# Optimization experiments

Hardware: AMD Instinct MI355X
Metric: run time of the kernel (lower is better)

## Reference

```python
import jax, jax.numpy as jnp
import numpy as np

B, T, D, H, E, TOPK = 4, 1024, 1024, 16, 8, 2
DH = D // H
FF = 4 * D
EPS = 1e-9


def setup_inputs() -> dict:
    key = jax.random.key(0)
    ks = jax.random.split(key, 8)
    s = 0.02
    return {
        "x": jax.random.normal(ks[0], (B, T, D), jnp.float32),
        "c": jax.random.normal(ks[1], (B, 1, D), jnp.float32),
        "ln1_w": jnp.ones((D,), jnp.float32),
        "w_qkv": jax.random.normal(ks[2], (3 * D, D), jnp.float32) * s,
        "w_proj": jax.random.normal(ks[3], (D, D), jnp.float32) * s,
        "ln2_w": jnp.ones((D,), jnp.float32),
        "router_w": jax.random.normal(ks[4], (E, D), jnp.float32) * s,
        "expert_w1": jax.random.normal(ks[5], (E, FF, D), jnp.float32) * s,
        "expert_w2": jax.random.normal(ks[6], (E, D, FF), jnp.float32) * s,
    }


def _layernorm(x, w):
    mu = jnp.mean(x, axis=-1, keepdims=True)
    var = jnp.mean(jnp.square(x - mu), axis=-1, keepdims=True)
    return (x - mu) * jax.lax.rsqrt(var + 1e-5) * w


def reference(x, c, ln1_w, w_qkv, w_proj, ln2_w, router_w, expert_w1, expert_w2):
    # --- causal self-attention with AdaLN-style additive conditioning ---
    h = _layernorm(x, ln1_w) + c                          # [B,T,D]
    qkv = jnp.einsum('btd,ed->bte', h, w_qkv)             # [B,T,3D]
    q, k, v = jnp.split(qkv, 3, axis=-1)
    q = q.reshape(B, T, H, DH).transpose(0, 2, 1, 3)       # [B,H,T,dh]
    k = k.reshape(B, T, H, DH).transpose(0, 2, 1, 3)
    v = v.reshape(B, T, H, DH).transpose(0, 2, 1, 3)
    scores = jnp.einsum('bhqd,bhkd->bhqk', q, k) / jnp.sqrt(jnp.float32(DH))
    causal = jnp.tril(jnp.ones((T, T), bool))
    scores = jnp.where(causal, scores, jnp.float32(-1e30))
    attn = jax.nn.softmax(scores, axis=-1)
    o = jnp.einsum('bhqk,bhkd->bhqd', attn, v)
    o = o.transpose(0, 2, 1, 3).reshape(B, T, D)
    x = x + jnp.einsum('btd,ed->bte', o, w_proj)

    # --- pre-MoE LayerNorm (note: module overwrites x with ln_2(x)) ---
    x = _layernorm(x, ln2_w)

    # --- router (non-cond path): linear, max-shift, softmax, eps clamp, top-k ---
    logits = jnp.einsum('btd,ed->bte', x, router_w)        # [B,T,E]
    logits = logits - jnp.max(logits, axis=-1, keepdims=True)
    probs = jax.nn.softmax(logits, axis=-1)
    probs = jnp.clip(probs + EPS, EPS, 1.0 - EPS)
    _, top_idx = jax.lax.top_k(probs, TOPK)                # [B,T,k]
    mask = jnp.sum(jax.nn.one_hot(top_idx, E, dtype=probs.dtype), axis=-2)  # [B,T,E]
    router_probs = mask * probs
    router_probs = router_probs / jnp.sum(router_probs, axis=-1, keepdims=True)

    # --- experts: GPT MLP per expert (fc -> GELU -> proj), combine by probs ---
    # Dense-compute form is mathematically identical: router_probs is 0 for
    # non-selected experts, so masked gather/scatter == weighted dense sum.
    hid = jax.nn.gelu(jnp.einsum('btd,efd->btef', x, expert_w1), approximate=False)
    expert_out = jnp.einsum('btef,edf->bted', hid, expert_w2)  # [B,T,E,D]
    next_states = jnp.einsum('bted,bte->btd', expert_out, router_probs)

    return x + next_states
```

## Files before the change

### kernel.cpp

```cpp
#include <hip/hip_runtime.h>
#include <cstdint>
#include <cstddef>


#define AS1 __attribute__((address_space(1)))
#define AS3 __attribute__((address_space(3)))

typedef unsigned short u16;
typedef __attribute__((ext_vector_type(8))) short short8;
typedef __attribute__((ext_vector_type(8))) _Float16 half8;
typedef __attribute__((ext_vector_type(4))) float f32x4;

constexpr int Bc = 4, Tc = 1024, Dc = 1024, Hc = 16, Ec = 8, FFc = 4096;
constexpr int Mtok = Bc * Tc;

constexpr size_t PS_WQKV = (size_t)3 * Dc * Dc;
constexpr size_t PS_WPROJ = (size_t)Dc * Dc;
constexpr size_t PS_H = (size_t)Mtok * Dc;

constexpr float LO_SCALE = 4096.0f;
constexpr float LO_INV = 1.0f / 4096.0f;

__device__ __forceinline__ u16 f2bf(float f) {
  unsigned u = __float_as_uint(f);
  u += 0x7fffu + ((u >> 16) & 1u);
  return (u16)(u >> 16);
}
__device__ __forceinline__ float bf2f(u16 v) { return __uint_as_float(((unsigned)v) << 16); }
__device__ __forceinline__ u16 f2h(float f) {
  _Float16 h = (_Float16)f;
  return *(u16*)&h;
}
__device__ __forceinline__ float h2f(u16 v) {
  _Float16 h = *(_Float16*)&v;
  return (float)h;
}
__device__ __forceinline__ float gelu_f(float v) {
  return 0.5f * v * (1.0f + erff(v * 0.70710678118654752440f));
}

__global__ __launch_bounds__(256) void cvt_fp16_kernel(const float* __restrict__ in,
                                                       u16* __restrict__ out, int n4) {
  int i = blockIdx.x * 256 + threadIdx.x;
  if (i >= n4) return;
  float4 v = reinterpret_cast<const float4*>(in)[i];
  uint2 o;
  o.x = (unsigned)f2h(v.x) | ((unsigned)f2h(v.y) << 16);
  o.y = (unsigned)f2h(v.z) | ((unsigned)f2h(v.w) << 16);
  reinterpret_cast<uint2*>(out)[i] = o;
}

__global__ __launch_bounds__(256) void split2h_kernel(const float* __restrict__ in,
                                                      u16* __restrict__ out,
                                                      size_t ps, int n4) {
  int i = blockIdx.x * 256 + threadIdx.x;
  if (i >= n4) return;
  float4 v = reinterpret_cast<const float4*>(in)[i];
  float a[4] = {v.x, v.y, v.z, v.w};
  unsigned h[4], lo[4];
#pragma unroll
  for (int j = 0; j < 4; ++j) {
    u16 hh = f2h(a[j]);
    float r = (a[j] - h2f(hh)) * LO_SCALE;
    h[j] = hh; lo[j] = f2h(r);
  }
  uint2 o0, o1;
  o0.x = h[0] | (h[1] << 16);   o0.y = h[2] | (h[3] << 16);
  o1.x = lo[0] | (lo[1] << 16); o1.y = lo[2] | (lo[3] << 16);
  const size_t base = (size_t)i * 4;
  *(uint2*)&out[base] = o0;
  *(uint2*)&out[ps + base] = o1;
}

__global__ __launch_bounds__(256) void ln1_kernel(const float* __restrict__ x,
                                                  const float* __restrict__ w,
                                                  const float* __restrict__ c,
                                                  u16* __restrict__ hp) {
  const int row = blockIdx.x, tid = threadIdx.x;
  const int b = row >> 10;
  const float4 v = reinterpret_cast<const float4*>(x + (size_t)row * Dc)[tid];
  __shared__ float red[256];
  red[tid] = v.x + v.y + v.z + v.w;
  __syncthreads();
  for (int s = 128; s > 0; s >>= 1) { if (tid < s) red[tid] += red[tid + s]; __syncthreads(); }
  const float mu = red[0] * (1.0f / Dc);
  __syncthreads();
  const float dx = v.x - mu, dy = v.y - mu, dz = v.z - mu, dw = v.w - mu;
  red[tid] = dx * dx + dy * dy + dz * dz + dw * dw;
  __syncthreads();
  for (int s = 128; s > 0; s >>= 1) { if (tid < s) red[tid] += red[tid + s]; __syncthreads(); }
  const float rs = rsqrtf(red[0] * (1.0f / Dc) + 1e-5f);
  const float4 wv = reinterpret_cast<const float4*>(w)[tid];
  const float4 cv = reinterpret_cast<const float4*>(c + (size_t)b * Dc)[tid];
  float a[4];
  a[0] = dx * rs * wv.x + cv.x; a[1] = dy * rs * wv.y + cv.y;
  a[2] = dz * rs * wv.z + cv.z; a[3] = dw * rs * wv.w + cv.w;
  unsigned h[4], lo[4];
#pragma unroll
  for (int j = 0; j < 4; ++j) {
    u16 hh = f2h(a[j]);
    float r = (a[j] - h2f(hh)) * LO_SCALE;
    h[j] = hh; lo[j] = f2h(r);
  }
  uint2 o0, o1;
  o0.x = h[0] | (h[1] << 16);   o0.y = h[2] | (h[3] << 16);
  o1.x = lo[0] | (lo[1] << 16); o1.y = lo[2] | (lo[3] << 16);
  const size_t base = (size_t)row * Dc + tid * 4;
  *(uint2*)&hp[base] = o0;
  *(uint2*)&hp[PS_H + base] = o1;
}

__global__ __launch_bounds__(256) void ln2_kernel(const float* __restrict__ xin,
                                                  const float* __restrict__ w,
                                                  float* __restrict__ xf,
                                                  u16* __restrict__ xb) {
  const int row = blockIdx.x, tid = threadIdx.x;
  const float4 v = reinterpret_cast<const float4*>(xin + (size_t)row * Dc)[tid];
  __shared__ float red[256];
  red[tid] = v.x + v.y + v.z + v.w;
  __syncthreads();
  for (int s = 128; s > 0; s >>= 1) { if (tid < s) red[tid] += red[tid + s]; __syncthreads(); }
  const float mu = red[0] * (1.0f / Dc);
  __syncthreads();
  const float dx = v.x - mu, dy = v.y - mu, dz = v.z - mu, dw = v.w - mu;
  red[tid] = dx * dx + dy * dy + dz * dz + dw * dw;
  __syncthreads();
  for (int s = 128; s > 0; s >>= 1) { if (tid < s) red[tid] += red[tid + s]; __syncthreads(); }
  const float rs = rsqrtf(red[0] * (1.0f / Dc) + 1e-5f);
  const float4 wv = reinterpret_cast<const float4*>(w)[tid];
  float4 ov;
  ov.x = dx * rs * wv.x; ov.y = dy * rs * wv.y; ov.z = dz * rs * wv.z; ov.w = dw * rs * wv.w;
  reinterpret_cast<float4*>(xf + (size_t)row * Dc)[tid] = ov;
  uint2 o;
  o.x = (unsigned)f2h(ov.x) | ((unsigned)f2h(ov.y) << 16);
  o.y = (unsigned)f2h(ov.z) | ((unsigned)f2h(ov.w) << 16);
  reinterpret_cast<uint2*>(xb + (size_t)row * Dc)[tid] = o;
}

__device__ __forceinline__ void stage4(const u16* a0, const u16* a1,
                                       const u16* b0, const u16* b1,
                                       u16* buf, int lds0) {
  __builtin_amdgcn_global_load_lds((AS1 void*)a0, (AS3 void*)(buf + lds0), 16, 0, 0);
  __builtin_amdgcn_global_load_lds((AS1 void*)a1, (AS3 void*)(buf + 2048 + lds0), 16, 0, 0);
  __builtin_amdgcn_global_load_lds((AS1 void*)b0, (AS3 void*)(buf + 4096 + lds0), 16, 0, 0);
  __builtin_amdgcn_global_load_lds((AS1 void*)b1, (AS3 void*)(buf + 6144 + lds0), 16, 0, 0);
}
__device__ __forceinline__ void stage8(const u16* ah0, const u16* ah1,
                                       const u16* al0, const u16* al1,
                                       const u16* bh0, const u16* bh1,
                                       const u16* bl0, const u16* bl1,
                                       u16* buf, int lds0) {
  __builtin_amdgcn_global_load_lds((AS1 void*)ah0, (AS3 void*)(buf + lds0), 16, 0, 0);
  __builtin_amdgcn_global_load_lds((AS1 void*)ah1, (AS3 void*)(buf + 2048 + lds0), 16, 0, 0);
  __builtin_amdgcn_global_load_lds((AS1 void*)al0, (AS3 void*)(buf + 4096 + lds0), 16, 0, 0);
  __builtin_amdgcn_global_load_lds((AS1 void*)al1, (AS3 void*)(buf + 6144 + lds0), 16, 0, 0);
  __builtin_amdgcn_global_load_lds((AS1 void*)bh0, (AS3 void*)(buf + 8192 + lds0), 16, 0, 0);
  __builtin_amdgcn_global_load_lds((AS1 void*)bh1, (AS3 void*)(buf + 10240 + lds0), 16, 0, 0);
  __builtin_amdgcn_global_load_lds((AS1 void*)bl0, (AS3 void*)(buf + 12288 + lds0), 16, 0, 0);
  __builtin_amdgcn_global_load_lds((AS1 void*)bl1, (AS3 void*)(buf + 14336 + lds0), 16, 0, 0);
}

__device__ __forceinline__ void gemm_f16_core(const u16* a0, const u16* a1,
                                              const u16* b0, const u16* b1,
                                              int K, u16* S, f32x4 acc[4][4]) {
  const int tid = threadIdx.x;
  const int lane = tid & 63;
  const int wave = tid >> 6;
  const int wm = (wave & 1) * 64;
  const int wn = (wave >> 1) * 64;
  const int frow = lane & 15;
  const int gs = ((lane >> 4) ^ ((frow >> 1) & 3)) * 8;
  int aoff[4], boff[4];
#pragma unroll
  for (int t = 0; t < 4; ++t) {
    aoff[t] = (wm + t * 16 + frow) * 32 + gs;
    boff[t] = 4096 + (wn + t * 16 + frow) * 32 + gs;
  }
  const int lds0 = tid * 8;
  stage4(a0, a1, b0, b1, S, lds0);
  a0 += 32; a1 += 32; b0 += 32; b1 += 32;
  int cur = 0;
  for (int k0 = 0; k0 < K; k0 += 32) {
    __syncthreads();
    if (k0 + 32 < K) {
      stage4(a0, a1, b0, b1, S + (cur ^ 1) * 8192, lds0);
      a0 += 32; a1 += 32; b0 += 32; b1 += 32;
    }
    const u16* As = S + cur * 8192;
    half8 af[4], bfr[4];
#pragma unroll
    for (int t = 0; t < 4; ++t) af[t] = *(const half8*)(As + aoff[t]);
#pragma unroll
    for (int t = 0; t < 4; ++t) bfr[t] = *(const half8*)(As + boff[t]);
#pragma unroll
    for (int mt = 0; mt < 4; ++mt)
#pragma unroll
      for (int nt = 0; nt < 4; ++nt)
        acc[mt][nt] = __builtin_amdgcn_mfma_f32_16x16x32_f16(af[mt], bfr[nt], acc[mt][nt], 0, 0, 0);
    cur ^= 1;
  }
}

__device__ __forceinline__ void gemm_f16s2_core(const u16* ah0, const u16* ah1,
                                                const u16* al0, const u16* al1,
                                                const u16* bh0, const u16* bh1,
                                                const u16* bl0, const u16* bl1,
                                                int K, u16* S,
                                                f32x4 acc0[4][4], f32x4 acc1[4][4]) {
  const int tid = threadIdx.x;
  const int lane = tid & 63;
  const int wave = tid >> 6;
  const int wm = (wave & 1) * 64;
  const int wn = (wave >> 1) * 64;
  const int frow = lane & 15;
  const int gs = ((lane >> 4) ^ ((frow >> 1) & 3)) * 8;
  int aoff[4], boff[4];
#pragma unroll
  for (int t = 0; t < 4; ++t) {
    aoff[t] = (wm + t * 16 + frow) * 32 + gs;
    boff[t] = 8192 + (wn + t * 16 + frow) * 32 + gs;
  }
  const int lds0 = tid * 8;
  stage8(ah0, ah1, al0, al1, bh0, bh1, bl0, bl1, S, lds0);
  ah0 += 32; ah1 += 32; al0 += 32; al1 += 32;
  bh0 += 32; bh1 += 32; bl0 += 32; bl1 += 32;
  int cur = 0;
  for (int k0 = 0; k0 < K; k0 += 32) {
    __syncthreads();
    if (k0 + 32 < K) {
      stage8(ah0, ah1, al0, al1, bh0, bh1, bl0, bl1, S + (cur ^ 1) * 16384, lds0);
      ah0 += 32; ah1 += 32; al0 += 32; al1 += 32;
      bh0 += 32; bh1 += 32; bl0 += 32; bl1 += 32;
    }
    const u16* Sb = S + cur * 16384;
    half8 ahf[4], bhf[4];
#pragma unroll
    for (int t = 0; t < 4; ++t) {
      ahf[t] = *(const half8*)(Sb + aoff[t]);
      bhf[t] = *(const half8*)(Sb + boff[t]);
    }
#pragma unroll
    for (int mt = 0; mt < 4; ++mt)
#pragma unroll
      for (int nt = 0; nt < 4; ++nt)
        acc0[mt][nt] = __builtin_amdgcn_mfma_f32_16x16x32_f16(ahf[mt], bhf[nt], acc0[mt][nt], 0, 0, 0);
    {
      half8 alf[4];
#pragma unroll
      for (int t = 0; t < 4; ++t) alf[t] = *(const half8*)(Sb + 4096 + aoff[t]);
#pragma unroll
      for (int mt = 0; mt < 4; ++mt)
#pragma unroll
        for (int nt = 0; nt < 4; ++nt)
          acc1[mt][nt] = __builtin_amdgcn_mfma_f32_16x16x32_f16(alf[mt], bhf[nt], acc1[mt][nt], 0, 0, 0);
    }
    {
      half8 blf[4];
#pragma unroll
      for (int t = 0; t < 4; ++t) blf[t] = *(const half8*)(Sb + 4096 + boff[t]);
#pragma unroll
      for (int mt = 0; mt < 4; ++mt)
#pragma unroll
        for (int nt = 0; nt < 4; ++nt)
          acc1[mt][nt] = __builtin_amdgcn_mfma_f32_16x16x32_f16(ahf[mt], blf[nt], acc1[mt][nt], 0, 0, 0);
    }
    cur ^= 1;
  }
}

__global__ __launch_bounds__(256) void gemm_qkv_kernel(const u16* __restrict__ A,
                                                       const u16* __restrict__ Bw,
                                                       float* __restrict__ Cout) {
  __shared__ u16 S[2 * 16384];
  const int bn = blockIdx.x, bm = blockIdx.y, tid = threadIdx.x;
  const int r = tid >> 2, kk = ((tid & 3) ^ ((r >> 1) & 3)) * 8;
  const u16* ah0 = A + (size_t)(bm * 128 + r) * 1024 + kk;
  const u16* ah1 = ah0 + (size_t)64 * 1024;
  const u16* bh0 = Bw + (size_t)(bn * 128 + r) * 1024 + kk;
  const u16* bh1 = bh0 + (size_t)64 * 1024;
  f32x4 acc0[4][4] = {}, acc1[4][4] = {};
  gemm_f16s2_core(ah0, ah1, ah0 + PS_H, ah1 + PS_H,
                  bh0, bh1, bh0 + PS_WQKV, bh1 + PS_WQKV,
                  1024, S, acc0, acc1);
  const int lane = tid & 63, wave = tid >> 6;
  const int wm = (wave & 1) * 64, wn = (wave >> 1) * 64;
  const int col = lane & 15, rb = (lane >> 4) * 4;
#pragma unroll
  for (int mt = 0; mt < 4; ++mt)
#pragma unroll
    for (int rr = 0; rr < 4; ++rr) {
      const int m = bm * 128 + wm + mt * 16 + rb + rr;
#pragma unroll
      for (int nt = 0; nt < 4; ++nt) {
        const int n = bn * 128 + wn + nt * 16 + col;
        Cout[(size_t)m * 3072 + n] = acc0[mt][nt][rr] + acc1[mt][nt][rr] * LO_INV;
      }
    }
}

__global__ __launch_bounds__(256) void gemm_proj_kernel(const u16* __restrict__ A,
                                                        const u16* __restrict__ Bw,
                                                        const float* __restrict__ xres,
                                                        float* __restrict__ xmid) {
  __shared__ u16 S[2 * 16384];
  const int bn = blockIdx.x, bm = blockIdx.y, tid = threadIdx.x;
  const int r = tid >> 2, kk = ((tid & 3) ^ ((r >> 1) & 3)) * 8;
  const u16* ah0 = A + (size_t)(bm * 128 + r) * 1024 + kk;
  const u16* ah1 = ah0 + (size_t)64 * 1024;
  const u16* bh0 = Bw + (size_t)(bn * 128 + r) * 1024 + kk;
  const u16* bh1 = bh0 + (size_t)64 * 1024;
  f32x4 acc0[4][4] = {}, acc1[4][4] = {};
  gemm_f16s2_core(ah0, ah1, ah0 + PS_H, ah1 + PS_H,
                  bh0, bh1, bh0 + PS_WPROJ, bh1 + PS_WPROJ,
                  1024, S, acc0, acc1);
  const int lane = tid & 63, wave = tid >> 6;
  const int wm = (wave & 1) * 64, wn = (wave >> 1) * 64;
  const int col = lane & 15, rb = (lane >> 4) * 4;
#pragma unroll
  for (int mt = 0; mt < 4; ++mt)
#pragma unroll
    for (int rr = 0; rr < 4; ++rr) {
      const int m = bm * 128 + wm + mt * 16 + rb + rr;
#pragma unroll
      for (int nt = 0; nt < 4; ++nt) {
        const int n = bn * 128 + wn + nt * 16 + col;
        xmid[(size_t)m * 1024 + n] =
            xres[(size_t)m * 1024 + n] + acc0[mt][nt][rr] + acc1[mt][nt][rr] * LO_INV;
      }
    }
}

__global__ __launch_bounds__(256, 3) void attn_mfma_kernel(const float* __restrict__ qkv,
                                                           float* __restrict__ obuf) {
  constexpr int KS = 72;
  constexpr int PSt = 68;
  __shared__ u16 Kh[64 * KS], Klo[64 * KS];
  __shared__ u16 Vh[64 * KS], Vlo[64 * KS];
  __shared__ u16 Ph[4][16 * PSt], Pl[4][16 * PSt];

  const int tid = threadIdx.x, lane = tid & 63, w = tid >> 6;
  const int lr = lane & 15, g = lane >> 4;
  const int bh = blockIdx.y, b = bh >> 4, h = bh & 15;
  const int blk = blockIdx.x;
  const int qrow = blk * 64 + w * 16 + lr;

  short8 qh[2], ql[2];
  {
    const float* qp = qkv + (size_t)(b * Tc + qrow) * 3072 + h * 64 + g * 8;
    const float4 f0 = *(const float4*)(qp);
    const float4 f1 = *(const float4*)(qp + 4);
    const float4 f2 = *(const float4*)(qp + 32);
    const float4 f3 = *(const float4*)(qp + 36);
    const float qq[16] = {f0.x, f0.y, f0.z, f0.w, f1.x, f1.y, f1.z, f1.w,
                          f2.x, f2.y, f2.z, f2.w, f3.x, f3.y, f3.z, f3.w};
#pragma unroll
    for (int s = 0; s < 2; ++s)
#pragma unroll
      for (int j = 0; j < 8; ++j) {
        const float v = qq[s * 8 + j] * 0.125f;
        const u16 hi = f2bf(v);
        qh[s][j] = (short)hi;
        ql[s][j] = (short)f2bf(v - bf2f(hi));
      }
  }

  const int tkl = (tid & 31) * 2;
  const int td0 = (tid >> 5) * 8;
  const float* kgb = qkv + (size_t)b * Tc * 3072 + 1024 + h * 64;
  const float* vgb = kgb + 1024;

  f32x4 oacc[4] = {};
  float mrun = -1e30f, lrun = 0.f;

  for (int c = 0; c <= blk; ++c) {
    const int k0 = c * 64;
    __syncthreads();
    {
      const float* kr0 = kgb + (size_t)(k0 + tkl) * 3072 + td0;
      const float* kr1 = kr0 + 3072;
      const float* vr0 = vgb + (size_t)(k0 + tkl) * 3072 + td0;
      const float* vr1 = vr0 + 3072;
      const float4 ka0 = *(const float4*)kr0, ka1 = *(const float4*)(kr0 + 4);
      const float4 kb0 = *(const float4*)kr1, kb1 = *(const float4*)(kr1 + 4);
      const float4 va0 = *(const float4*)vr0, va1 = *(const float4*)(vr0 + 4);
      const float4 vb0 = *(const float4*)vr1, vb1 = *(const float4*)(vr1 + 4);
      const float ka[8] = {ka0.x, ka0.y, ka0.z, ka0.w, ka1.x, ka1.y, ka1.z, ka1.w};
      const float kb[8] = {kb0.x, kb0.y, kb0.z, kb0.w, kb1.x, kb1.y, kb1.z, kb1.w};
      const float va[8] = {va0.x, va0.y, va0.z, va0.w, va1.x, va1.y, va1.z, va1.w};
      const float vb[8] = {vb0.x, vb0.y, vb0.z, vb0.w, vb1.x, vb1.y, vb1.z, vb1.w};
      short8 kh0, kl0, kh1, kl1;
#pragma unroll
      for (int j = 0; j < 8; ++j) {
        const u16 h0 = f2bf(ka[j]); kh0[j] = (short)h0; kl0[j] = (short)f2bf(ka[j] - bf2f(h0));
        const u16 h1 = f2bf(kb[j]); kh1[j] = (short)h1; kl1[j] = (short)f2bf(kb[j] - bf2f(h1));
      }
      *(short8*)(Kh + tkl * KS + td0) = kh0;
      *(short8*)(Kh + (tkl + 1) * KS + td0) = kh1;
      *(short8*)(Klo + tkl * KS + td0) = kl0;
      *(short8*)(Klo + (tkl + 1) * KS + td0) = kl1;
#pragma unroll
      for (int i = 0; i < 8; ++i) {
        const u16 h0 = f2bf(va[i]); const u16 l0 = f2bf(va[i] - bf2f(h0));
        const u16 h1 = f2bf(vb[i]); const u16 l1 = f2bf(vb[i] - bf2f(h1));
        *(unsigned*)(Vh + (td0 + i) * KS + tkl) = (unsigned)h0 | ((unsigned)h1 << 16);
        *(unsigned*)(Vlo + (td0 + i) * KS + tkl) = (unsigned)l0 | ((unsigned)l1 << 16);
      }
    }
    __syncthreads();

    f32x4 sacc[4] = {};
#pragma unroll
    for (int kt = 0; kt < 4; ++kt) {
      const u16* kap = Kh + (kt * 16 + lr) * KS + g * 8;
      const u16* klp = Klo + (kt * 16 + lr) * KS + g * 8;
      const short8 ah0 = *(const short8*)kap;
      const short8 ah1 = *(const short8*)(kap + 32);
      const short8 al0 = *(const short8*)klp;
      const short8 al1 = *(const short8*)(klp + 32);
      sacc[kt] = __builtin_amdgcn_mfma_f32_16x16x32_bf16(ah0, qh[0], sacc[kt], 0, 0, 0);
      sacc[kt] = __builtin_amdgcn_mfma_f32_16x16x32_bf16(al0, qh[0], sacc[kt], 0, 0, 0);
      sacc[kt] = __builtin_amdgcn_mfma_f32_16x16x32_bf16(ah0, ql[0], sacc[kt], 0, 0, 0);
      sacc[kt] = __builtin_amdgcn_mfma_f32_16x16x32_bf16(ah1, qh[1], sacc[kt], 0, 0, 0);
      sacc[kt] = __builtin_amdgcn_mfma_f32_16x16x32_bf16(al1, qh[1], sacc[kt], 0, 0, 0);
      sacc[kt] = __builtin_amdgcn_mfma_f32_16x16x32_bf16(ah1, ql[1], sacc[kt], 0, 0, 0);
    }

    if (c == blk) {
#pragma unroll
      for (int kt = 0; kt < 4; ++kt)
#pragma unroll
        for (int r = 0; r < 4; ++r)
          if (k0 + kt * 16 + g * 4 + r > qrow) sacc[kt][r] = -1e30f;
    }

    float mt = -1e30f;
#pragma unroll
    for (int kt = 0; kt < 4; ++kt)
#pragma unroll
      for (int r = 0; r < 4; ++r) mt = fmaxf(mt, sacc[kt][r]);
    mt = fmaxf(mt, __shfl_xor(mt, 16));
    mt = fmaxf(mt, __shfl_xor(mt, 32));
    const float mnew = fmaxf(mrun, mt);
    const float alpha = __expf(mrun - mnew);
    float psum = 0.f;
    u16* php = Ph[w] + lr * PSt;
    u16* plp = Pl[w] + lr * PSt;
#pragma unroll
    for (int kt = 0; kt < 4; ++kt) {
      u16 hh[4], ll[4];
#pragma unroll
      for (int r = 0; r < 4; ++r) {
        const float p = __expf(sacc[kt][r] - mnew);
        psum += p;
        hh[r] = f2bf(p);
        ll[r] = f2bf(p - bf2f(hh[r]));
      }
      uint2 wh, wl;
      wh.x = (unsigned)hh[0] | ((unsigned)hh[1] << 16);
      wh.y = (unsigned)hh[2] | ((unsigned)hh[3] << 16);
      wl.x = (unsigned)ll[0] | ((unsigned)ll[1] << 16);
      wl.y = (unsigned)ll[2] | ((unsigned)ll[3] << 16);
      *(uint2*)(php + kt * 16 + g * 4) = wh;
      *(uint2*)(plp + kt * 16 + g * 4) = wl;
    }
    psum += __shfl_xor(psum, 16);
    psum += __shfl_xor(psum, 32);
    mrun = mnew;
    lrun = lrun * alpha + psum;
#pragma unroll
    for (int dt = 0; dt < 4; ++dt) {
      oacc[dt][0] *= alpha; oacc[dt][1] *= alpha;
      oacc[dt][2] *= alpha; oacc[dt][3] *= alpha;
    }
    __syncthreads();

    const short8 pbh0 = *(const short8*)(php + g * 8);
    const short8 pbh1 = *(const short8*)(php + 32 + g * 8);
    const short8 pbl0 = *(const short8*)(plp + g * 8);
    const short8 pbl1 = *(const short8*)(plp + 32 + g * 8);
#pragma unroll
    for (int dt = 0; dt < 4; ++dt) {
      const u16* vap = Vh + (dt * 16 + lr) * KS + g * 8;
      const u16* vlp2 = Vlo + (dt * 16 + lr) * KS + g * 8;
      const short8 vh0 = *(const short8*)vap;
      const short8 vh1 = *(const short8*)(vap + 32);
      const short8 vl0 = *(const short8*)vlp2;
      const short8 vl1 = *(const short8*)(vlp2 + 32);
      oacc[dt] = __builtin_amdgcn_mfma_f32_16x16x32_bf16(vh0, pbh0, oacc[dt], 0, 0, 0);
      oacc[dt] = __builtin_amdgcn_mfma_f32_16x16x32_bf16(vl0, pbh0, oacc[dt], 0, 0, 0);
      oacc[dt] = __builtin_amdgcn_mfma_f32_16x16x32_bf16(vh0, pbl0, oacc[dt], 0, 0, 0);
      oacc[dt] = __builtin_amdgcn_mfma_f32_16x16x32_bf16(vh1, pbh1, oacc[dt], 0, 0, 0);
      oacc[dt] = __builtin_amdgcn_mfma_f32_16x16x32_bf16(vl1, pbh1, oacc[dt], 0, 0, 0);
      oacc[dt] = __builtin_amdgcn_mfma_f32_16x16x32_bf16(vh1, pbl1, oacc[dt], 0, 0, 0);
    }
  }

  const float invl = 1.0f / lrun;
  float* ob = obuf + (size_t)(b * Tc + qrow) * 1024 + h * 64;
#pragma unroll
  for (int dt = 0; dt < 4; ++dt) {
    float4 o4;
    o4.x = oacc[dt][0] * invl; o4.y = oacc[dt][1] * invl;
    o4.z = oacc[dt][2] * invl; o4.w = oacc[dt][3] * invl;
    *(float4*)(ob + dt * 16 + g * 4) = o4;
  }
}

__global__ __launch_bounds__(256) void router_kernel(const float* __restrict__ x2,
                                                     const float* __restrict__ rw,
                                                     int* __restrict__ cnt,
                                                     int* __restrict__ tok,
                                                     float* __restrict__ wt) {
  __shared__ float xr[1024];
  __shared__ float part[8][32];
  __shared__ float lg[8];
  const int row = blockIdx.x, tid = threadIdx.x;
  reinterpret_cast<float4*>(xr)[tid] = reinterpret_cast<const float4*>(x2 + (size_t)row * Dc)[tid];
  __syncthreads();
  const int e = tid >> 5, j = tid & 31;
  float p = 0.f;
  for (int d = j; d < Dc; d += 32) p += xr[d] * rw[e * Dc + d];
  part[e][j] = p;
  __syncthreads();
  if (tid < 8) {
    float s = 0.f;
    for (int q = 0; q < 32; ++q) s += part[tid][q];
    lg[tid] = s;
  }
  __syncthreads();
  if (tid == 0) {
    int i0 = 0;
    for (int q = 1; q < 8; ++q) if (lg[q] > lg[i0]) i0 = q;
    int i1 = (i0 == 0) ? 1 : 0;
    for (int q = 0; q < 8; ++q) if (q != i0 && lg[q] > lg[i1]) i1 = q;
    float mx = lg[0];
    for (int q = 1; q < 8; ++q) mx = fmaxf(mx, lg[q]);
    float ex[8], s = 0.f;
    for (int q = 0; q < 8; ++q) { ex[q] = expf(lg[q] - mx); s += ex[q]; }
    const float inv = 1.f / s;
    float p0v = fminf(fmaxf(ex[i0] * inv + 1e-9f, 1e-9f), 1.f - 1e-9f);
    float p1v = fminf(fmaxf(ex[i1] * inv + 1e-9f, 1e-9f), 1.f - 1e-9f);
    const float sw = 1.f / (p0v + p1v);
    int p0 = atomicAdd(&cnt[i0], 1);
    tok[i0 * Mtok + p0] = row; wt[i0 * Mtok + p0] = p0v * sw;
    int p1 = atomicAdd(&cnt[i1], 1);
    tok[i1 * Mtok + p1] = row; wt[i1 * Mtok + p1] = p1v * sw;
  }
}

__global__ __launch_bounds__(256) void gemm_e1_kernel(const u16* __restrict__ x2b,
                                                      const u16* __restrict__ w1,
                                                      const int* __restrict__ cnt,
                                                      const int* __restrict__ tok,
                                                      u16* __restrict__ hid) {
  const int bn = blockIdx.x;
  const int e = blockIdx.y >> 5, it = blockIdx.y & 31;
  const int n_e = cnt[e];
  if (it * 128 >= n_e) return;
  int offs = 0;
  for (int q = 0; q < 8; ++q) offs += (q < e) ? cnt[q] : 0;
  __shared__ u16 S[2 * 8192];
  const int tid = threadIdx.x;
  const int r = tid >> 2, kk = ((tid & 3) ^ ((r >> 1) & 3)) * 8;
  const int i0 = it * 128 + r, i1 = i0 + 64;
  const int t0 = tok[e * Mtok + ((i0 < n_e) ? i0 : (n_e - 1))];
  const int t1 = tok[e * Mtok + ((i1 < n_e) ? i1 : (n_e - 1))];
  const u16* a0 = x2b + (size_t)t0 * 1024 + kk;
  const u16* a1 = x2b + (size_t)t1 * 1024 + kk;
  const u16* b0 = w1 + (size_t)e * FFc * Dc + (size_t)(bn * 128 + r) * 1024 + kk;
  const u16* b1 = b0 + (size_t)64 * 1024;
  f32x4 acc[4][4] = {};
  gemm_f16_core(a0, a1, b0, b1, 1024, S, acc);
  const int lane = tid & 63, wave = tid >> 6;
  const int wm = (wave & 1) * 64, wn = (wave >> 1) * 64;
  const int col = lane & 15, rb = (lane >> 4) * 4;
#pragma unroll
  for (int mt = 0; mt < 4; ++mt)
#pragma unroll
    for (int rr = 0; rr < 4; ++rr) {
      const int i = it * 128 + wm + mt * 16 + rb + rr;
      if (i < n_e) {
        const size_t hrow = (size_t)(offs + i) * FFc;
#pragma unroll
        for (int nt = 0; nt < 4; ++nt) {
          const int n = bn * 128 + wn + nt * 16 + col;
          hid[hrow + n] = f2h(gelu_f(acc[mt][nt][rr]));
        }
      }
    }
}

__global__ __launch_bounds__(256) void gemm_e2_kernel(const u16* __restrict__ hid,
                                                      const u16* __restrict__ w2,
                                                      const int* __restrict__ cnt,
                                                      const int* __restrict__ tok,
                                                      const float* __restrict__ wt,
                                                      float* __restrict__ out) {
  const int bn = blockIdx.x;
  const int e = blockIdx.y >> 5, it = blockIdx.y & 31;
  const int n_e = cnt[e];
  if (it * 128 >= n_e) return;
  int offs = 0;
  for (int q = 0; q < 8; ++q) offs += (q < e) ? cnt[q] : 0;
  __shared__ u16 S[2 * 8192];
  const int tid = threadIdx.x;
  const int r = tid >> 2, kk = ((tid & 3) ^ ((r >> 1) & 3)) * 8;
  const int i0 = it * 128 + r, i1 = i0 + 64;
  const int ri0 = offs + ((i0 < n_e) ? i0 : (n_e - 1));
  const int ri1 = offs + ((i1 < n_e) ? i1 : (n_e - 1));
  const u16* a0 = hid + (size_t)ri0 * FFc + kk;
  const u16* a1 = hid + (size_t)ri1 * FFc + kk;
  const u16* b0 = w2 + (size_t)e * Dc * FFc + (size_t)(bn * 128 + r) * FFc + kk;
  const u16* b1 = b0 + (size_t)64 * FFc;
  f32x4 acc[4][4] = {};
  gemm_f16_core(a0, a1, b0, b1, FFc, S, acc);
  const int lane = tid & 63, wave = tid >> 6;
  const int wm = (wave & 1) * 64, wn = (wave >> 1) * 64;
  const int col = lane & 15, rb = (lane >> 4) * 4;
#pragma unroll
  for (int mt = 0; mt < 4; ++mt)
#pragma unroll
    for (int rr = 0; rr < 4; ++rr) {
      const int i = it * 128 + wm + mt * 16 + rb + rr;
      if (i < n_e) {
        const int tk = tok[e * Mtok + i];
        const float wgt = wt[e * Mtok + i];
#pragma unroll
        for (int nt = 0; nt < 4; ++nt) {
          const int n = bn * 128 + wn + nt * 16 + col;
          atomicAdd(&out[(size_t)tk * 1024 + n], wgt * acc[mt][nt][rr]);
        }
      }
    }
}

constexpr size_t OFF_WQKV3 = 0;
constexpr size_t OFF_WPROJ3 = 18874368;
constexpr size_t OFF_W1 = 25165824;
constexpr size_t OFF_W2 = 92274688;
constexpr size_t OFF_HPL = 159383552;
constexpr size_t OFF_QKV = 184549376;
constexpr size_t OFF_OF = 234881024;
constexpr size_t OFF_X2 = 251658240;
constexpr size_t OFF_CNT = 260046848;
constexpr size_t OFF_TOK = OFF_CNT + 256;
constexpr size_t OFF_WTL = OFF_TOK + (size_t)Ec * Mtok * 4;

extern "C" void kernel_launch(void* const* d_in, const int* in_sizes, int n_in,
                              void* d_out, int out_size, void* d_ws, size_t ws_size,
                              hipStream_t stream) {
  const float* x = (const float*)d_in[0];
  const float* c = (const float*)d_in[1];
  const float* ln1_w = (const float*)d_in[2];
  const float* w_qkv = (const float*)d_in[3];
  const float* w_proj = (const float*)d_in[4];
  const float* ln2_w = (const float*)d_in[5];
  const float* router_w = (const float*)d_in[6];
  const float* ew1 = (const float*)d_in[7];
  const float* ew2 = (const float*)d_in[8];
  float* out = (float*)d_out;
  char* ws = (char*)d_ws;

  u16* wqkv2 = (u16*)(ws + OFF_WQKV3);
  u16* wproj2 = (u16*)(ws + OFF_WPROJ3);
  u16* w1_h = (u16*)(ws + OFF_W1);
  u16* w2_h = (u16*)(ws + OFF_W2);
  u16* hpl = (u16*)(ws + OFF_HPL);
  float* qkvf = (float*)(ws + OFF_QKV);
  float* of = (float*)(ws + OFF_OF);
  u16* x2_h = (u16*)(ws + OFF_X2);
  u16* hid_h = (u16*)(ws + OFF_QKV);
  int* cnt = (int*)(ws + OFF_CNT);
  int* tok = (int*)(ws + OFF_TOK);
  float* wtl = (float*)(ws + OFF_WTL);

  split2h_kernel<<<(3 * Dc * Dc / 4 + 255) / 256, 256, 0, stream>>>(w_qkv, wqkv2, PS_WQKV, 3 * Dc * Dc / 4);
  split2h_kernel<<<(Dc * Dc / 4 + 255) / 256, 256, 0, stream>>>(w_proj, wproj2, PS_WPROJ, Dc * Dc / 4);
  {
    int n4 = Ec * FFc * Dc / 4;
    cvt_fp16_kernel<<<(n4 + 255) / 256, 256, 0, stream>>>(ew1, w1_h, n4);
    cvt_fp16_kernel<<<(n4 + 255) / 256, 256, 0, stream>>>(ew2, w2_h, n4);
  }
  ln1_kernel<<<Mtok, 256, 0, stream>>>(x, ln1_w, c, hpl);
  gemm_qkv_kernel<<<dim3(24, 32), 256, 0, stream>>>(hpl, wqkv2, qkvf);
  attn_mfma_kernel<<<dim3(Tc / 64, Bc * Hc), 256, 0, stream>>>(qkvf, of);
  split2h_kernel<<<(Mtok * Dc / 4 + 255) / 256, 256, 0, stream>>>(of, hpl, PS_H, Mtok * Dc / 4);
  gemm_proj_kernel<<<dim3(8, 32), 256, 0, stream>>>(hpl, wproj2, x, of);
  ln2_kernel<<<Mtok, 256, 0, stream>>>(of, ln2_w, out, x2_h);
  (void)hipMemsetAsync(cnt, 0, Ec * sizeof(int), stream);
  router_kernel<<<Mtok, 256, 0, stream>>>(out, router_w, cnt, tok, wtl);
  gemm_e1_kernel<<<dim3(32, 256), 256, 0, stream>>>(x2_h, w1_h, cnt, tok, hid_h);
  gemm_e2_kernel<<<dim3(8, 256), 256, 0, stream>>>(hid_h, w2_h, cnt, tok, wtl, out);
}
```

Measured before the change: 943.5 us.

## Triple-buffer LDS in GEMM cores with vmcnt-based waits instead of syncthreads

Converts the double-buffered global_load_lds GEMM mainloops (plain f16 and split-f16) to a three-stage ring with two tiles in flight. Each iteration waits only for the oldest tile via s_waitcnt vmcnt(N) plus a barrier, rather than a full __syncthreads, so global loads can overlap more compute. LDS per block grows by half, which may lower occupancy for the QKV/proj kernels that now use 96KB.

Measured after the change: 946.7 us. No clear change (+0.3%).

```diff
diff --git a/kernel.cpp b/kernel.cpp
--- a/kernel.cpp
+++ b/kernel.cpp
@@ -160,6 +160,26 @@
   __builtin_amdgcn_global_load_lds((AS1 void*)bl1, (AS3 void*)(buf + 14336 + lds0), 16, 0, 0);
 }
 
+#define PIPE_WAIT(N)                                        \
+  asm volatile("s_waitcnt vmcnt(" #N ")" ::: "memory");     \
+  __builtin_amdgcn_s_barrier();                             \
+  asm volatile("" ::: "memory");                            \
+  __builtin_amdgcn_sched_barrier(0);
+
+__device__ __forceinline__ void gemm_f16_compute(const u16* Sb, const int aoff[4],
+                                                 const int boff[4], f32x4 acc[4][4]) {
+  half8 af[4], bfr[4];
+#pragma unroll
+  for (int t = 0; t < 4; ++t) af[t] = *(const half8*)(Sb + aoff[t]);
+#pragma unroll
+  for (int t = 0; t < 4; ++t) bfr[t] = *(const half8*)(Sb + boff[t]);
+#pragma unroll
+  for (int mt = 0; mt < 4; ++mt)
+#pragma unroll
+    for (int nt = 0; nt < 4; ++nt)
+      acc[mt][nt] = __builtin_amdgcn_mfma_f32_16x16x32_f16(af[mt], bfr[nt], acc[mt][nt], 0, 0, 0);
+}
+
 __device__ __forceinline__ void gemm_f16_core(const u16* a0, const u16* a1,
                                               const u16* b0, const u16* b1,
                                               int K, u16* S, f32x4 acc[4][4]) {
@@ -177,27 +197,59 @@
     boff[t] = 4096 + (wn + t * 16 + frow) * 32 + gs;
   }
   const int lds0 = tid * 8;
+  const int NT = K >> 5;
   stage4(a0, a1, b0, b1, S, lds0);
   a0 += 32; a1 += 32; b0 += 32; b1 += 32;
+  stage4(a0, a1, b0, b1, S + 8192, lds0);
+  a0 += 32; a1 += 32; b0 += 32; b1 += 32;
   int cur = 0;
-  for (int k0 = 0; k0 < K; k0 += 32) {
-    __syncthreads();
-    if (k0 + 32 < K) {
-      stage4(a0, a1, b0, b1, S + (cur ^ 1) * 8192, lds0);
+  for (int t = 0; t < NT - 1; ++t) {
+    PIPE_WAIT(4)
+    if (t + 2 < NT) {
+      int nxt = cur + 2; if (nxt >= 3) nxt -= 3;
+      stage4(a0, a1, b0, b1, S + nxt * 8192, lds0);
       a0 += 32; a1 += 32; b0 += 32; b1 += 32;
     }
-    const u16* As = S + cur * 8192;
-    half8 af[4], bfr[4];
-#pragma unroll
-    for (int t = 0; t < 4; ++t) af[t] = *(const half8*)(As + aoff[t]);
-#pragma unroll
-    for (int t = 0; t < 4; ++t) bfr[t] = *(const half8*)(As + boff[t]);
+    gemm_f16_compute(S + cur * 8192, aoff, boff, acc);
+    ++cur; if (cur >= 3) cur = 0;
+  }
+  PIPE_WAIT(0)
+  gemm_f16_compute(S + cur * 8192, aoff, boff, acc);
+}
+
+__device__ __forceinline__ void gemm_f16s2_compute(const u16* Sb, const int aoff[4],
+                                                   const int boff[4],
+                                                   f32x4 acc0[4][4], f32x4 acc1[4][4]) {
+  half8 ahf[4], bhf[4];
+#pragma unroll
+  for (int t = 0; t < 4; ++t) {
+    ahf[t] = *(const half8*)(Sb + aoff[t]);
+    bhf[t] = *(const half8*)(Sb + boff[t]);
+  }
+#pragma unroll
+  for (int mt = 0; mt < 4; ++mt)
+#pragma unroll
+    for (int nt = 0; nt < 4; ++nt)
+      acc0[mt][nt] = __builtin_amdgcn_mfma_f32_16x16x32_f16(ahf[mt], bhf[nt], acc0[mt][nt], 0, 0, 0);
+  {
+    half8 alf[4];
+#pragma unroll
+    for (int t = 0; t < 4; ++t) alf[t] = *(const half8*)(Sb + 4096 + aoff[t]);
 #pragma unroll
     for (int mt = 0; mt < 4; ++mt)
 #pragma unroll
       for (int nt = 0; nt < 4; ++nt)
-        acc[mt][nt] = __builtin_amdgcn_mfma_f32_16x16x32_f16(af[mt], bfr[nt], acc[mt][nt], 0, 0, 0);
-    cur ^= 1;
+        acc1[mt][nt] = __builtin_amdgcn_mfma_f32_16x16x32_f16(alf[mt], bhf[nt], acc1[mt][nt], 0, 0, 0);
+  }
+  {
+    half8 blf[4];
+#pragma unroll
+    for (int t = 0; t < 4; ++t) blf[t] = *(const half8*)(Sb + 4096 + boff[t]);
+#pragma unroll
+    for (int mt = 0; mt < 4; ++mt)
+#pragma unroll
+      for (int nt = 0; nt < 4; ++nt)
+        acc1[mt][nt] = __builtin_amdgcn_mfma_f32_16x16x32_f16(ahf[mt], blf[nt], acc1[mt][nt], 0, 0, 0);
   }
 }
 
@@ -221,57 +273,33 @@
     boff[t] = 8192 + (wn + t * 16 + frow) * 32 + gs;
   }
   const int lds0 = tid * 8;
+  const int NT = K >> 5;
   stage8(ah0, ah1, al0, al1, bh0, bh1, bl0, bl1, S, lds0);
   ah0 += 32; ah1 += 32; al0 += 32; al1 += 32;
   bh0 += 32; bh1 += 32; bl0 += 32; bl1 += 32;
+  stage8(ah0, ah1, al0, al1, bh0, bh1, bl0, bl1, S + 16384, lds0);
+  ah0 += 32; ah1 += 32; al0 += 32; al1 += 32;
+  bh0 += 32; bh1 += 32; bl0 += 32; bl1 += 32;
   int cur = 0;
-  for (int k0 = 0; k0 < K; k0 += 32) {
-    __syncthreads();
-    if (k0 + 32 < K) {
-      stage8(ah0, ah1, al0, al1, bh0, bh1, bl0, bl1, S + (cur ^ 1) * 16384, lds0);
+  for (int t = 0; t < NT - 1; ++t) {
+    PIPE_WAIT(8)
+    if (t + 2 < NT) {
+      int nxt = cur + 2; if (nxt >= 3) nxt -= 3;
+      stage8(ah0, ah1, al0, al1, bh0, bh1, bl0, bl1, S + nxt * 16384, lds0);
       ah0 += 32; ah1 += 32; al0 += 32; al1 += 32;
       bh0 += 32; bh1 += 32; bl0 += 32; bl1 += 32;
     }
-    const u16* Sb = S + cur * 16384;
-    half8 ahf[4], bhf[4];
-#pragma unroll
-    for (int t = 0; t < 4; ++t) {
-      ahf[t] = *(const half8*)(Sb + aoff[t]);
-      bhf[t] = *(const half8*)(Sb + boff[t]);
-    }
-#pragma unroll
-    for (int mt = 0; mt < 4; ++mt)
-#pragma unroll
-      for (int nt = 0; nt < 4; ++nt)
-        acc0[mt][nt] = __builtin_amdgcn_mfma_f32_16x16x32_f16(ahf[mt], bhf[nt], acc0[mt][nt], 0, 0, 0);
-    {
-      half8 alf[4];
-#pragma unroll
-      for (int t = 0; t < 4; ++t) alf[t] = *(const half8*)(Sb + 4096 + aoff[t]);
-#pragma unroll
-      for (int mt = 0; mt < 4; ++mt)
-#pragma unroll
-        for (int nt = 0; nt < 4; ++nt)
-          acc1[mt][nt] = __builtin_amdgcn_mfma_f32_16x16x32_f16(alf[mt], bhf[nt], acc1[mt][nt], 0, 0, 0);
-    }
-    {
-      half8 blf[4];
-#pragma unroll
-      for (int t = 0; t < 4; ++t) blf[t] = *(const half8*)(Sb + 4096 + boff[t]);
-#pragma unroll
-      for (int mt = 0; mt < 4; ++mt)
-#pragma unroll
-        for (int nt = 0; nt < 4; ++nt)
-          acc1[mt][nt] = __builtin_amdgcn_mfma_f32_16x16x32_f16(ahf[mt], blf[nt], acc1[mt][nt], 0, 0, 0);
-    }
-    cur ^= 1;
-  }
+    gemm_f16s2_compute(S + cur * 16384, aoff, boff, acc0, acc1);
+    ++cur; if (cur >= 3) cur = 0;
+  }
+  PIPE_WAIT(0)
+  gemm_f16s2_compute(S + cur * 16384, aoff, boff, acc0, acc1);
 }
 
 __global__ __launch_bounds__(256) void gemm_qkv_kernel(const u16* __restrict__ A,
                                                        const u16* __restrict__ Bw,
                                                        float* __restrict__ Cout) {
-  __shared__ u16 S[2 * 16384];
+  __shared__ u16 S[3 * 16384];
   const int bn = blockIdx.x, bm = blockIdx.y, tid = threadIdx.x;
   const int r = tid >> 2, kk = ((tid & 3) ^ ((r >> 1) & 3)) * 8;
   const u16* ah0 = A + (size_t)(bm * 128 + r) * 1024 + kk;
@@ -302,7 +330,7 @@
                                                         const u16* __restrict__ Bw,
                                                         const float* __restrict__ xres,
                                                         float* __restrict__ xmid) {
-  __shared__ u16 S[2 * 16384];
+  __shared__ u16 S[3 * 16384];
   const int bn = blockIdx.x, bm = blockIdx.y, tid = threadIdx.x;
   const int r = tid >> 2, kk = ((tid & 3) ^ ((r >> 1) & 3)) * 8;
   const u16* ah0 = A + (size_t)(bm * 128 + r) * 1024 + kk;
@@ -559,7 +587,7 @@
   if (it * 128 >= n_e) return;
   int offs = 0;
   for (int q = 0; q < 8; ++q) offs += (q < e) ? cnt[q] : 0;
-  __shared__ u16 S[2 * 8192];
+  __shared__ u16 S[3 * 8192];
   const int tid = threadIdx.x;
   const int r = tid >> 2, kk = ((tid & 3) ^ ((r >> 1) & 3)) * 8;
   const int i0 = it * 128 + r, i1 = i0 + 64;
@@ -602,7 +630,7 @@
   if (it * 128 >= n_e) return;
   int offs = 0;
   for (int q = 0; q < 8; ++q) offs += (q < e) ? cnt[q] : 0;
-  __shared__ u16 S[2 * 8192];
+  __shared__ u16 S[3 * 8192];
   const int tid = threadIdx.x;
   const int r = tid >> 2, kk = ((tid & 3) ^ ((r >> 1) & 3)) * 8;
   const int i0 = it * 128 + r, i1 = i0 + 64;
```
